# Kernel optimization log

Hardware: AMD Instinct MI355X
Metric: run time of the kernel (lower is better)

The kernel has to match this reference:

```python
import jax, jax.numpy as jnp
import numpy as np

N = 100000      # number of nodes/edges
R = 32          # relation_dim
I = 256         # input_dim
O = 256         # output_dim


def setup_inputs() -> dict:
    key = jax.random.key(0)
    k1, k2, k3, k4 = jax.random.split(key, 4)
    x = jax.random.normal(k1, (N, I), dtype=jnp.float32)
    # relation weights per node (e.g. soft relation assignment), non-negative
    edge_attr = jax.random.uniform(k2, (N, R), dtype=jnp.float32)
    # xavier_uniform-style init for W [R, O, I] and b [R, O]
    a_w = float(np.sqrt(6.0 / (I + O)))
    W = jax.random.uniform(k3, (R, O, I), dtype=jnp.float32, minval=-a_w, maxval=a_w)
    a_b = float(np.sqrt(6.0 / (R + O)))
    b = jax.random.uniform(k4, (R, O), dtype=jnp.float32, minval=-a_b, maxval=a_b)
    return {"x": x, "edge_attr": edge_attr, "W": W, "b": b}


def reference(x, edge_attr, W, b):
    # y[n,o] = sum_r edge_attr[n,r] * (W[r] @ x[n])[o] + (edge_attr @ b)[n,o]
    # Stream over the small relation axis, accumulating into [N, O];
    # avoids materializing the naive [N, R, O] intermediate.
    def body(acc, s):
        W_r, e_r = s                      # W_r: [O, I], e_r: [N]
        acc = acc + e_r[:, None] * (x @ W_r.T)  # [N, O]
        return acc, None

    y0 = edge_attr @ b                    # bias term: [N, R] @ [R, O] -> [N, O]
    y, _ = jax.lax.scan(body, y0, (W, edge_attr.T))
    return y
```

## Files before the change

kernel.cpp:

```cpp
#include <hip/hip_runtime.h>
#include <hip/hip_bf16.h>


typedef __attribute__((ext_vector_type(4))) float f32x4;
typedef __attribute__((ext_vector_type(8))) short short8;
typedef __attribute__((ext_vector_type(8))) unsigned short ushort8;

#define R_DIM 32
#define I_DIM 256
#define O_DIM 256
#define KW    8192
#define KEXT  8256
#define BM    128
#define BNB   128
#define BK    64
#define NT    (KEXT / BK)
#define NTHR  512

__device__ __forceinline__ unsigned short f2bf(float f) {
  unsigned u = __builtin_bit_cast(unsigned, f);
  u += 0x7FFFu + ((u >> 16) & 1u);
  return (unsigned short)(u >> 16);
}

__device__ __forceinline__ unsigned pk2(float a, float b) {
  __hip_bfloat162 h = __float22bfloat162_rn(make_float2(a, b));
  unsigned u;
  __builtin_memcpy(&u, &h, sizeof(u));
  return u;
}

__device__ __forceinline__ void gld_lds16(const void* g, void* l) {
  __builtin_amdgcn_global_load_lds(
      (const __attribute__((address_space(1))) unsigned int*)g,
      (__attribute__((address_space(3))) unsigned int*)l, 16, 0, 0);
}

__global__ void prep_w(const float* __restrict__ W, const float* __restrict__ b,
                       unsigned short* __restrict__ Wb) {
  const int id = blockIdx.x * 256 + threadIdx.x;
  const int o  = id / (KEXT / 4);
  const int k4 = (id - o * (KEXT / 4)) * 4;
  float v[4];
  if (k4 < KW) {
    const int r  = k4 & 31;
    const int ih = (k4 >> 5) & 1;
    const int il = k4 >> 6;
    const int i  = 128 * ih + il;
#pragma unroll
    for (int j = 0; j < 4; ++j)
      v[j] = W[((size_t)((r + j) * O_DIM + o)) * I_DIM + i];
  } else {
    const int kk = k4 - KW;
#pragma unroll
    for (int j = 0; j < 4; ++j)
      v[j] = (kk + j < R_DIM) ? b[(kk + j) * O_DIM + o] : 0.f;
  }
  uint2 pk;
  pk.x = pk2(v[0], v[1]);
  pk.y = pk2(v[2], v[3]);
  *(uint2*)&Wb[(size_t)o * KEXT + k4] = pk;
}

__global__ __launch_bounds__(NTHR)
__attribute__((amdgpu_waves_per_eu(4)))
void lkg2b(
    const float* __restrict__ x, const float* __restrict__ e,
    const unsigned short* __restrict__ Wb, float* __restrict__ out, int Ntot) {
  __shared__ unsigned short Al[2][BM * BK];
  __shared__ unsigned short Bl[3][BNB * BK];

  const int tid  = threadIdx.x;
  const int lane = tid & 63;
  const int w    = tid >> 6;
  const int wr   = w >> 2;
  const int wc   = w & 3;
  const int l15  = lane & 15;
  const int sx   = (l15 & 7) << 4;
  const int kb0  = (lane >> 4) << 4;

  const int mi = (int)blockIdx.x >> 1;
  const int ni = (int)blockIdx.x & 1;
  const int m0 = mi * BM;
  const unsigned short* WbN = Wb + (size_t)(ni * BNB) * KEXT;

  const int srow = tid >> 2;
  const int q    = tid & 3;
  const int ih   = q >> 1;
  const int gr   = min(m0 + srow, Ntot - 1);

  const int bro = lane >> 3;
  const int bch = (lane & 7) ^ bro;

  float er[16];
#pragma unroll
  for (int p = 0; p < 4; ++p) {
    const float4 ev = *(const float4*)&e[(size_t)gr * R_DIM + (q & 1) * 16 + p * 4];
    er[p * 4 + 0] = ev.x; er[p * 4 + 1] = ev.y;
    er[p * 4 + 2] = ev.z; er[p * 4 + 3] = ev.w;
  }
  const float* xrow = x + (size_t)gr * I_DIM + ih * 128;
  const float biasx = (ih == 0) ? 1.f : 0.f;

  f32x4 acc[4][2];
#pragma unroll
  for (int a = 0; a < 4; ++a)
#pragma unroll
    for (int c = 0; c < 2; ++c) acc[a][c] = (f32x4){0.f, 0.f, 0.f, 0.f};

  auto issueB2 = [&](unsigned short* Bd, int t2) {
    const size_t k0 = (size_t)t2 * BK;
#pragma unroll
    for (int g = 0; g < 2; ++g)
      gld_lds16(WbN + (size_t)(w * 16 + g * 8 + bro) * KEXT + k0 + bch * 8,
                Bd + (w * 16 + g * 8) * BK);
  };
  auto stageA = [&](unsigned short* Ad, float xs) {
    char* rowp = (char*)(Ad + srow * BK);
    const int sw = (srow & 7) << 4;
    const int qb = q * 32;
    uint4 wv;
    wv.x = pk2(xs * er[0], xs * er[1]);
    wv.y = pk2(xs * er[2], xs * er[3]);
    wv.z = pk2(xs * er[4], xs * er[5]);
    wv.w = pk2(xs * er[6], xs * er[7]);
    *(uint4*)(rowp + ((qb + 0) ^ sw)) = wv;
    uint4 wv2;
    wv2.x = pk2(xs * er[8],  xs * er[9]);
    wv2.y = pk2(xs * er[10], xs * er[11]);
    wv2.z = pk2(xs * er[12], xs * er[13]);
    wv2.w = pk2(xs * er[14], xs * er[15]);
    *(uint4*)(rowp + ((qb + 16) ^ sw)) = wv2;
  };
  auto rdA = [&](const unsigned short* Ab, int ks, int fr) -> short8 {
    const int row = wr * 64 + fr * 16 + l15;
    return *(const short8*)((const char*)Ab + row * 128 + ((ks * 64 + kb0) ^ sx));
  };
  auto rdB = [&](const unsigned short* Bb, int ks, int fc) -> short8 {
    const int row = wc * 32 + fc * 16 + l15;
    return *(const short8*)((const char*)Bb + row * 128 + ((ks * 64 + kb0) ^ sx));
  };

  auto tileF = [&](int t, float xs, int mode, int apar, int cb) {
    const unsigned short* Ac = Al[apar];
    unsigned short*       Aw = Al[apar ^ 1];
    const unsigned short* Bc = Bl[cb];
    unsigned short*       Bw = Bl[cb >= 1 ? cb - 1 : 2];

    short8 af[4], bf[2];

#pragma unroll
    for (int fr = 0; fr < 4; ++fr) af[fr] = rdA(Ac, 0, fr);
#pragma unroll
    for (int fc = 0; fc < 2; ++fc) bf[fc] = rdB(Bc, 0, fc);
    if (mode & 2) issueB2(Bw, t + 2);
    __builtin_amdgcn_s_barrier();
    asm volatile("s_waitcnt lgkmcnt(0)" ::: "memory");
    __builtin_amdgcn_s_setprio(1);
#pragma unroll
    for (int fr = 0; fr < 4; ++fr)
#pragma unroll
      for (int fc = 0; fc < 2; ++fc)
        acc[fr][fc] = __builtin_amdgcn_mfma_f32_16x16x32_bf16(af[fr], bf[fc],
                                                              acc[fr][fc], 0, 0, 0);
    __builtin_amdgcn_s_setprio(0);
    __builtin_amdgcn_s_barrier();

#pragma unroll
    for (int fr = 0; fr < 4; ++fr) af[fr] = rdA(Ac, 1, fr);
#pragma unroll
    for (int fc = 0; fc < 2; ++fc) bf[fc] = rdB(Bc, 1, fc);
    if (mode & 1) stageA(Aw, xs);
    asm volatile("s_waitcnt lgkmcnt(0)" ::: "memory");
    if (mode & 2) {
      asm volatile("s_waitcnt vmcnt(2)" ::: "memory");
    } else {
      asm volatile("s_waitcnt vmcnt(0)" ::: "memory");
    }
    __builtin_amdgcn_s_barrier();
    __builtin_amdgcn_s_setprio(1);
#pragma unroll
    for (int fr = 0; fr < 4; ++fr)
#pragma unroll
      for (int fc = 0; fc < 2; ++fc)
        acc[fr][fc] = __builtin_amdgcn_mfma_f32_16x16x32_bf16(af[fr], bf[fc],
                                                              acc[fr][fc], 0, 0, 0);
    __builtin_amdgcn_s_setprio(0);
    __builtin_amdgcn_s_barrier();
  };

  float4 xv = *(const float4*)xrow;
  stageA(Al[0], xv.x);
  issueB2(Bl[0], 0);
  issueB2(Bl[1], 1);
  asm volatile("s_waitcnt lgkmcnt(0)" ::: "memory");
  asm volatile("s_waitcnt vmcnt(2)" ::: "memory");
  __builtin_amdgcn_s_barrier();

  int cb = 0;
  for (int u = 0; u < 32; ++u) {
    float4 xvn = xv;
    if (u < 31) xvn = *(const float4*)(xrow + (u + 1) * 4);
    const int t0 = u * 4;
    tileF(t0 + 0, xv.y, 3, 0, cb); cb = (cb == 2) ? 0 : cb + 1;
    tileF(t0 + 1, xv.z, 3, 1, cb); cb = (cb == 2) ? 0 : cb + 1;
    tileF(t0 + 2, xv.w, 3, 0, cb); cb = (cb == 2) ? 0 : cb + 1;
    if (u < 31) {
      tileF(t0 + 3, xvn.x, 3, 1, cb);
    } else {
      tileF(t0 + 3, biasx, 1, 1, cb);
    }
    cb = (cb == 2) ? 0 : cb + 1;
    xv = xvn;
  }
  tileF(128, 0.f, 0, 0, cb);

#pragma unroll
  for (int fr = 0; fr < 4; ++fr) {
    const int r0 = m0 + wr * 64 + fr * 16 + (lane >> 4) * 4;
#pragma unroll
    for (int j = 0; j < 4; ++j) {
      const int rr = r0 + j;
      if (rr < Ntot) {
#pragma unroll
        for (int fc = 0; fc < 2; ++fc) {
          const int col = ni * BNB + wc * 32 + fc * 16 + l15;
          out[(size_t)rr * O_DIM + col] = acc[fr][fc][j];
        }
      }
    }
  }
}

__global__ __launch_bounds__(256) void lkg_fb(
    const float* __restrict__ x, const float* __restrict__ e,
    const float* __restrict__ Wf, const float* __restrict__ bf32,
    float* __restrict__ out, int Ntot) {
  const int FBK = 64;
  const int FNT = (KW + 64) / FBK;
  __shared__ unsigned short Alds[128 * 64];
  __shared__ unsigned short Blds[256 * 64];

  const int tid = threadIdx.x, lane = tid & 63, wid = tid >> 6;
  const int wr = wid >> 1, wc = wid & 1, l15 = lane & 15, lk8 = (lane >> 4) * 8;
  const int m0 = (int)blockIdx.x * 128;
  const int srow = tid >> 1, skq = (tid & 1) * 32;
  const int gr = min(m0 + srow, Ntot - 1);

  f32x4 acc[4][8];
#pragma unroll
  for (int a = 0; a < 4; ++a)
#pragma unroll
    for (int c = 0; c < 8; ++c) acc[a][c] = (f32x4){0.f, 0.f, 0.f, 0.f};

  for (int t = 0; t < FNT; ++t) {
    const int k0 = t * FBK;
    float av[32];
    if (k0 < KW) {
      const int r = k0 >> 8, i0 = k0 & 255;
      const float ev = e[(size_t)gr * R_DIM + r];
#pragma unroll
      for (int p = 0; p < 8; ++p) {
        const float4 xvv = *(const float4*)&x[(size_t)gr * I_DIM + i0 + skq + p * 4];
        av[p * 4 + 0] = xvv.x * ev; av[p * 4 + 1] = xvv.y * ev;
        av[p * 4 + 2] = xvv.z * ev; av[p * 4 + 3] = xvv.w * ev;
      }
    } else {
#pragma unroll
      for (int s2 = 0; s2 < 32; ++s2) {
        const int kk = skq + s2;
        av[s2] = (kk < R_DIM) ? e[(size_t)gr * R_DIM + kk] : 0.f;
      }
    }
    const int bo = tid;
    if (k0 < KW) {
      const int r = k0 >> 8, i0 = k0 & 255;
#pragma unroll
      for (int h = 0; h < 4; ++h) {
        float bv[16];
#pragma unroll
        for (int p = 0; p < 4; ++p) {
          const float4 wv =
              *(const float4*)&Wf[((size_t)(r * O_DIM + bo)) * I_DIM + i0 + h * 16 + p * 4];
          bv[p * 4 + 0] = wv.x; bv[p * 4 + 1] = wv.y;
          bv[p * 4 + 2] = wv.z; bv[p * 4 + 3] = wv.w;
        }
#pragma unroll
        for (int g2 = 0; g2 < 2; ++g2) {
          ushort8 pw;
#pragma unroll
          for (int j = 0; j < 8; ++j) pw[j] = f2bf(bv[g2 * 8 + j]);
          *(ushort8*)&Blds[bo * FBK + h * 16 + g2 * 8] = pw;
        }
      }
    } else {
#pragma unroll
      for (int h = 0; h < 8; ++h) {
        ushort8 pw;
#pragma unroll
        for (int j = 0; j < 8; ++j) {
          const int kk = h * 8 + j;
          pw[j] = (kk < R_DIM) ? f2bf(bf32[kk * O_DIM + bo]) : (unsigned short)0;
        }
        *(ushort8*)&Blds[bo * FBK + h * 8] = pw;
      }
    }
#pragma unroll
    for (int h = 0; h < 4; ++h) {
      ushort8 pw;
#pragma unroll
      for (int j = 0; j < 8; ++j) pw[j] = f2bf(av[h * 8 + j]);
      *(ushort8*)&Alds[srow * FBK + skq + h * 8] = pw;
    }
    __syncthreads();
#pragma unroll
    for (int ks = 0; ks < 2; ++ks) {
      short8 af[4]; short8 bfr[8];
#pragma unroll
      for (int fr = 0; fr < 4; ++fr)
        af[fr] = *(const short8*)&Alds[(wr * 64 + fr * 16 + l15) * FBK + ks * 32 + lk8];
#pragma unroll
      for (int fc = 0; fc < 8; ++fc)
        bfr[fc] = *(const short8*)&Blds[(wc * 128 + fc * 16 + l15) * FBK + ks * 32 + lk8];
#pragma unroll
      for (int fr = 0; fr < 4; ++fr)
#pragma unroll
        for (int fc = 0; fc < 8; ++fc)
          acc[fr][fc] =
              __builtin_amdgcn_mfma_f32_16x16x32_bf16(af[fr], bfr[fc], acc[fr][fc], 0, 0, 0);
    }
    __syncthreads();
  }
#pragma unroll
  for (int fr = 0; fr < 4; ++fr) {
    const int r0 = m0 + wr * 64 + fr * 16 + (lane >> 4) * 4;
#pragma unroll
    for (int fc = 0; fc < 8; ++fc) {
      const int col = wc * 128 + fc * 16 + l15;
#pragma unroll
      for (int j = 0; j < 4; ++j) {
        const int rr = r0 + j;
        if (rr < Ntot) out[(size_t)rr * O_DIM + col] = acc[fr][fc][j];
      }
    }
  }
}

extern "C" void kernel_launch(void* const* d_in, const int* in_sizes, int n_in,
                              void* d_out, int out_size, void* d_ws, size_t ws_size,
                              hipStream_t stream) {
  const float* x = (const float*)d_in[0];
  const float* e = (const float*)d_in[1];
  const float* W = (const float*)d_in[2];
  const float* b = (const float*)d_in[3];
  float* out = (float*)d_out;
  const int Ntot = in_sizes[0] / I_DIM;

  const size_t wb_bytes = (size_t)O_DIM * KEXT * sizeof(unsigned short);
  if (ws_size >= wb_bytes) {
    unsigned short* Wb = (unsigned short*)d_ws;
    prep_w<<<(O_DIM * (KEXT / 4)) / 256, 256, 0, stream>>>(W, b, Wb);
    const int nb = ((Ntot + BM - 1) / BM) * 2;
    lkg2b<<<nb, NTHR, 0, stream>>>(x, e, Wb, out, Ntot);
  } else {
    lkg_fb<<<(Ntot + 127) / 128, 256, 0, stream>>>(x, e, W, b, out, Ntot);
  }
}
```

Baseline: 519.6 us.

## Switch to 32x32x16 MFMA and one barrier per K-tile pipeline

Replaces the 16x16x32 bf16 MFMA tiling (4x2 fragments per wave) with 32x32x16 MFMA using two 32x32 accumulators per wave. This cuts LDS fragment reads per MFMA, since B is shared across both A fragments. The per-tile schedule also collapses from two half-tiles, each with its own barrier pair, into a single loop: issue the next B prefetch and stage A, compute, then wait and take one barrier. The goal is fewer LDS reads and barriers. The cost is that A staging and the next B load are no longer interleaved with separate barrier-guarded compute phases, so latency hiding could change.

```diff
diff --git a/kernel.cpp b/kernel.cpp
--- a/kernel.cpp
+++ b/kernel.cpp
@@ -3,6 +3,7 @@
 
 
 typedef __attribute__((ext_vector_type(4))) float f32x4;
+typedef __attribute__((ext_vector_type(16))) float f32x16;
 typedef __attribute__((ext_vector_type(8))) short short8;
 typedef __attribute__((ext_vector_type(8))) unsigned short ushort8;
 
@@ -64,7 +65,7 @@
 
 __global__ __launch_bounds__(NTHR)
 __attribute__((amdgpu_waves_per_eu(4)))
-void lkg2b(
+void lkg17(
     const float* __restrict__ x, const float* __restrict__ e,
     const unsigned short* __restrict__ Wb, float* __restrict__ out, int Ntot) {
   __shared__ unsigned short Al[2][BM * BK];
@@ -75,9 +76,8 @@
   const int w    = tid >> 6;
   const int wr   = w >> 2;
   const int wc   = w & 3;
-  const int l15  = lane & 15;
-  const int sx   = (l15 & 7) << 4;
-  const int kb0  = (lane >> 4) << 4;
+  const int l31  = lane & 31;
+  const int sx   = (lane & 7) << 4;
 
   const int mi = (int)blockIdx.x >> 1;
   const int ni = (int)blockIdx.x & 1;
@@ -102,11 +102,9 @@
   const float* xrow = x + (size_t)gr * I_DIM + ih * 128;
   const float biasx = (ih == 0) ? 1.f : 0.f;
 
-  f32x4 acc[4][2];
-#pragma unroll
-  for (int a = 0; a < 4; ++a)
-#pragma unroll
-    for (int c = 0; c < 2; ++c) acc[a][c] = (f32x4){0.f, 0.f, 0.f, 0.f};
+  f32x16 acc0, acc1;
+#pragma unroll
+  for (int j = 0; j < 16; ++j) { acc0[j] = 0.f; acc1[j] = 0.f; }
 
   auto issueB2 = [&](unsigned short* Bd, int t2) {
     const size_t k0 = (size_t)t2 * BK;
@@ -132,61 +130,21 @@
     wv2.w = pk2(xs * er[14], xs * er[15]);
     *(uint4*)(rowp + ((qb + 16) ^ sw)) = wv2;
   };
-  auto rdA = [&](const unsigned short* Ab, int ks, int fr) -> short8 {
-    const int row = wr * 64 + fr * 16 + l15;
-    return *(const short8*)((const char*)Ab + row * 128 + ((ks * 64 + kb0) ^ sx));
-  };
-  auto rdB = [&](const unsigned short* Bb, int ks, int fc) -> short8 {
-    const int row = wc * 32 + fc * 16 + l15;
-    return *(const short8*)((const char*)Bb + row * 128 + ((ks * 64 + kb0) ^ sx));
-  };
-
-  auto tileF = [&](int t, float xs, int mode, int apar, int cb) {
-    const unsigned short* Ac = Al[apar];
-    unsigned short*       Aw = Al[apar ^ 1];
-    const unsigned short* Bc = Bl[cb];
-    unsigned short*       Bw = Bl[cb >= 1 ? cb - 1 : 2];
-
-    short8 af[4], bf[2];
-
-#pragma unroll
-    for (int fr = 0; fr < 4; ++fr) af[fr] = rdA(Ac, 0, fr);
-#pragma unroll
-    for (int fc = 0; fc < 2; ++fc) bf[fc] = rdB(Bc, 0, fc);
-    if (mode & 2) issueB2(Bw, t + 2);
-    __builtin_amdgcn_s_barrier();
-    asm volatile("s_waitcnt lgkmcnt(0)" ::: "memory");
-    __builtin_amdgcn_s_setprio(1);
-#pragma unroll
-    for (int fr = 0; fr < 4; ++fr)
-#pragma unroll
-      for (int fc = 0; fc < 2; ++fc)
-        acc[fr][fc] = __builtin_amdgcn_mfma_f32_16x16x32_bf16(af[fr], bf[fc],
-                                                              acc[fr][fc], 0, 0, 0);
-    __builtin_amdgcn_s_setprio(0);
-    __builtin_amdgcn_s_barrier();
-
-#pragma unroll
-    for (int fr = 0; fr < 4; ++fr) af[fr] = rdA(Ac, 1, fr);
-#pragma unroll
-    for (int fc = 0; fc < 2; ++fc) bf[fc] = rdB(Bc, 1, fc);
-    if (mode & 1) stageA(Aw, xs);
-    asm volatile("s_waitcnt lgkmcnt(0)" ::: "memory");
-    if (mode & 2) {
-      asm volatile("s_waitcnt vmcnt(2)" ::: "memory");
-    } else {
-      asm volatile("s_waitcnt vmcnt(0)" ::: "memory");
-    }
-    __builtin_amdgcn_s_barrier();
-    __builtin_amdgcn_s_setprio(1);
-#pragma unroll
-    for (int fr = 0; fr < 4; ++fr)
-#pragma unroll
-      for (int fc = 0; fc < 2; ++fc)
-        acc[fr][fc] = __builtin_amdgcn_mfma_f32_16x16x32_bf16(af[fr], bf[fc],
-                                                              acc[fr][fc], 0, 0, 0);
-    __builtin_amdgcn_s_setprio(0);
-    __builtin_amdgcn_s_barrier();
+  auto compute = [&](const unsigned short* Ab, const unsigned short* Bb) {
+#pragma unroll
+    for (int ks = 0; ks < 4; ++ks) {
+      const int kb = (ks * 32 + ((lane >> 5) << 4)) ^ sx;
+      const short8 a0 =
+          *(const short8*)((const char*)Ab + (wr * 64 + l31) * 128 + kb);
+      const short8 a1 =
+          *(const short8*)((const char*)Ab + (wr * 64 + 32 + l31) * 128 + kb);
+      const short8 bq =
+          *(const short8*)((const char*)Bb + (wc * 32 + l31) * 128 + kb);
+      __builtin_amdgcn_s_setprio(1);
+      acc0 = __builtin_amdgcn_mfma_f32_32x32x16_bf16(a0, bq, acc0, 0, 0, 0);
+      acc1 = __builtin_amdgcn_mfma_f32_32x32x16_bf16(a1, bq, acc1, 0, 0, 0);
+      __builtin_amdgcn_s_setprio(0);
+    }
   };
 
   float4 xv = *(const float4*)xrow;
@@ -201,33 +159,40 @@
   for (int u = 0; u < 32; ++u) {
     float4 xvn = xv;
     if (u < 31) xvn = *(const float4*)(xrow + (u + 1) * 4);
-    const int t0 = u * 4;
-    tileF(t0 + 0, xv.y, 3, 0, cb); cb = (cb == 2) ? 0 : cb + 1;
-    tileF(t0 + 1, xv.z, 3, 1, cb); cb = (cb == 2) ? 0 : cb + 1;
-    tileF(t0 + 2, xv.w, 3, 0, cb); cb = (cb == 2) ? 0 : cb + 1;
-    if (u < 31) {
-      tileF(t0 + 3, xvn.x, 3, 1, cb);
-    } else {
-      tileF(t0 + 3, biasx, 1, 1, cb);
-    }
-    cb = (cb == 2) ? 0 : cb + 1;
+#pragma unroll
+    for (int s = 0; s < 4; ++s) {
+      const int t  = u * 4 + s;
+      const int tn = t + 1;
+      unsigned short* An = Al[tn & 1];
+      unsigned short* Bn = Bl[cb >= 1 ? cb - 1 : 2];
+      if (t < 127) issueB2(Bn, t + 2);
+      if (s == 0)      stageA(An, xv.y);
+      else if (s == 1) stageA(An, xv.z);
+      else if (s == 2) stageA(An, xv.w);
+      else if (u < 31) stageA(An, xvn.x);
+      else             stageA(An, biasx);
+      compute(Al[t & 1], Bl[cb]);
+      asm volatile("s_waitcnt lgkmcnt(0)" ::: "memory");
+      if (t < 127) {
+        asm volatile("s_waitcnt vmcnt(2)" ::: "memory");
+      } else {
+        asm volatile("s_waitcnt vmcnt(0)" ::: "memory");
+      }
+      __builtin_amdgcn_s_barrier();
+      cb = (cb == 2) ? 0 : cb + 1;
+    }
     xv = xvn;
   }
-  tileF(128, 0.f, 0, 0, cb);
-
-#pragma unroll
-  for (int fr = 0; fr < 4; ++fr) {
-    const int r0 = m0 + wr * 64 + fr * 16 + (lane >> 4) * 4;
-#pragma unroll
-    for (int j = 0; j < 4; ++j) {
-      const int rr = r0 + j;
-      if (rr < Ntot) {
-#pragma unroll
-        for (int fc = 0; fc < 2; ++fc) {
-          const int col = ni * BNB + wc * 32 + fc * 16 + l15;
-          out[(size_t)rr * O_DIM + col] = acc[fr][fc][j];
-        }
-      }
+  compute(Al[0], Bl[cb]);
+
+  const int col = ni * BNB + wc * 32 + l31;
+#pragma unroll
+  for (int a = 0; a < 2; ++a) {
+#pragma unroll
+    for (int rg = 0; rg < 16; ++rg) {
+      const int rr = m0 + wr * 64 + a * 32 + (rg & 3) + 8 * (rg >> 2) + 4 * (lane >> 5);
+      if (rr < Ntot)
+        out[(size_t)rr * O_DIM + col] = a ? acc1[rg] : acc0[rg];
     }
   }
 }
@@ -361,7 +326,7 @@
     unsigned short* Wb = (unsigned short*)d_ws;
     prep_w<<<(O_DIM * (KEXT / 4)) / 256, 256, 0, stream>>>(W, b, Wb);
     const int nb = ((Ntot + BM - 1) / BM) * 2;
-    lkg2b<<<nb, NTHR, 0, stream>>>(x, e, Wb, out, Ntot);
+    lkg17<<<nb, NTHR, 0, stream>>>(x, e, Wb, out, Ntot);
   } else {
     lkg_fb<<<(Ntot + 127) / 128, 256, 0, stream>>>(x, e, W, b, out, Ntot);
   }
```

After: 579.4 us. +11.5%, slower.
